# Performance work log

Measured on AMD Instinct MI355X. Metric: run time of the kernel, lower is better.

## Reference

```python
import math
import jax, jax.numpy as jnp
import numpy as np

B, R, L_, K_, U_ = 64, 32, 64, 16, 4
DIMS = [2 * K_ * U_, 256, 256, K_]  # [input_dim] + hidden_dim + [output_dim]
BN_EPS = 1e-5


def _uniform_param(key, out_dim, in_dim):
    ini = math.sqrt(3.0 / out_dim / in_dim)
    return jax.random.uniform(key, (out_dim, in_dim), jnp.float32, -ini, ini)


def setup_inputs() -> dict:
    key = jax.random.key(0)
    ks = jax.random.split(key, 16)
    inp = {
        "Hhat_real": jax.random.normal(ks[0], (B, R, L_, K_, U_), jnp.float32),
        "Hhat_imag": jax.random.normal(ks[1], (B, R, L_, K_, U_), jnp.float32),
        "Vhat": jax.random.normal(ks[2], (B, R, L_, K_, U_), jnp.float32),
    }
    kidx = 3
    for i in range(len(DIMS) - 1):
        inp[f"P1_{i}"] = _uniform_param(ks[kidx], DIMS[i + 1], DIMS[i]); kidx += 1
        inp[f"P2_{i}"] = _uniform_param(ks[kidx], DIMS[i + 1], DIMS[i]); kidx += 1
        if i != len(DIMS) - 2:  # BN only on non-final layers
            inp[f"bn_w{i}"] = jnp.ones((DIMS[i + 1],), jnp.float32)
            inp[f"bn_b{i}"] = jnp.zeros((DIMS[i + 1],), jnp.float32)
    inp["nbrOfRealizations"] = R
    inp["L"] = L_
    inp["K"] = K_
    inp["U"] = U_
    return inp


def _layer(A, P1, P2, bn_w, bn_b, relu):
    # A: [N, C_in, L]
    A1 = jnp.einsum('oc,ncl->nol', P1, A)                       # [N, C_out, L]
    A2 = jnp.einsum('oc,nc->no', P2, A.mean(-1))[:, :, None]    # [N, C_out, 1]
    A = A1 + 0.1 * A2
    if relu:
        A = jax.nn.relu(A)
    if bn_w is not None:
        # BatchNorm1d (training mode): normalize over (N, L) per channel
        mu = A.mean(axis=(0, 2), keepdims=True)
        var = A.var(axis=(0, 2), keepdims=True)
        A = (A - mu) * jax.lax.rsqrt(var + BN_EPS) * bn_w[None, :, None] + bn_b[None, :, None]
    return A


def reference(Hhat_real, Hhat_imag, Vhat,
              P1_0, P2_0, bn_w0, bn_b0,
              P1_1, P2_1, bn_w1, bn_b1,
              P1_2, P2_2,
              nbrOfRealizations, L, K, U):
    Bsz = Hhat_real.shape[0]
    N = Bsz * nbrOfRealizations

    def prep(X):
        # view(N,1,L,K,U).transpose(2,3).transpose(3,4) -> [N,1,K,U,L]
        return jnp.transpose(X.reshape(N, 1, L, K, U), (0, 1, 3, 4, 2))

    A = jnp.concatenate([prep(Hhat_real), prep(Hhat_imag)], axis=1).reshape(N, 2 * K * U, L)
    A = _layer(A, P1_0, P2_0, bn_w0, bn_b0, relu=True)
    A = _layer(A, P1_1, P2_1, bn_w1, bn_b1, relu=True)
    A = _layer(A, P1_2, P2_2, None, None, relu=False)

    Phat_u1 = jnp.transpose(A.reshape(Bsz, nbrOfRealizations, K, L), (0, 1, 3, 2))  # [B,R,L,K]
    nrm = jnp.linalg.norm(Phat_u1, axis=2, keepdims=True)                            # [B,R,1,K]
    Phat_u = Phat_u1 / nrm * jnp.float32(math.sqrt(L))
    Fhat_u = Vhat.reshape(Bsz, nbrOfRealizations, L, K, U) * Phat_u[..., None]
    return Fhat_u
```

## Files before the change

### kernel.cpp

```cpp
#include <hip/hip_runtime.h>

typedef unsigned short ushort_t;
typedef unsigned int uint_t;

typedef short bf16x8 __attribute__((ext_vector_type(8)));
typedef float f32x4 __attribute__((ext_vector_type(4)));
#define MFMA16(a, b, c) __builtin_amdgcn_mfma_f32_16x16x32_bf16(a, b, c, 0, 0, 0)

__device__ __forceinline__ float bf2f(uint_t u) { return __uint_as_float(u << 16); }
__device__ __forceinline__ ushort_t f2bf(float f) {
  uint_t x = __float_as_uint(f);
  return (ushort_t)((x + 0x7fffu + ((x >> 16) & 1u)) >> 16);
}
__device__ __forceinline__ uint_t cvtpk(float lo, float hi) {
  uint_t r;
  asm("v_cvt_pk_bf16_f32 %0, %1, %2" : "=v"(r) : "v"(lo), "v"(hi));
  return r;
}
__device__ __forceinline__ void gload_lds16(const void* g, void* l) {
  __builtin_amdgcn_global_load_lds(
      (const __attribute__((address_space(1))) unsigned int*)g,
      (__attribute__((address_space(3))) unsigned int*)l, 16, 0, 0);
}

#define NBATCH 2048

__global__ __launch_bounds__(256) void cvt_w0_kernel(
    const float* __restrict__ P1_0, ushort_t* __restrict__ W0bf)
{
  int i = blockIdx.x * 256 + threadIdx.x;
  W0bf[i] = f2bf(P1_0[i]);
}

__global__ __launch_bounds__(256) void pre0_kernel(
    const float* __restrict__ Hr, const float* __restrict__ Hi,
    const float* __restrict__ P2_0, float* __restrict__ V20)
{
  __shared__ float r[4][128];
  __shared__ float hm[128];
  const int t = threadIdx.x, n = blockIdx.x;
  const int q = t >> 6;
  const int c = (2 * t) & 127;
  const int cc = c & 63;
  const float* src = ((c < 64) ? Hr : Hi) + (size_t)n * 4096 + cc;
  float s0 = 0.f, s1 = 0.f;
  #pragma unroll
  for (int i = 0; i < 16; i++) {
    int l = 4 * i + q;
    float2 x = *(const float2*)(src + l * 64);
    s0 += x.x; s1 += x.y;
  }
  r[q][c] = s0; r[q][c + 1] = s1;
  __syncthreads();
  if (t < 128) hm[t] = (r[0][t] + r[1][t] + r[2][t] + r[3][t]) * (1.0f / 64.0f);
  __syncthreads();
  const float4* pw = (const float4*)(P2_0 + t * 128);
  float s = 0.f;
  #pragma unroll 8
  for (int c4 = 0; c4 < 32; c4++) {
    float4 p = pw[c4];
    s = fmaf(p.x, hm[4 * c4 + 0], s);
    s = fmaf(p.y, hm[4 * c4 + 1], s);
    s = fmaf(p.z, hm[4 * c4 + 2], s);
    s = fmaf(p.w, hm[4 * c4 + 3], s);
  }
  V20[n * 256 + t] = 0.1f * s;
}

__global__ __launch_bounds__(256) void layer0_mfma_kernel(
    const float* __restrict__ Hr, const float* __restrict__ Hi,
    const ushort_t* __restrict__ W0bf, const float* __restrict__ V20,
    ushort_t* __restrict__ Z, float* __restrict__ partA, float* __restrict__ partB)
{
  __shared__ ushort_t lds[64 * 264];
  const int t = threadIdx.x, n = blockIdx.x;
  const int lane = t & 63, w = t >> 6, r16 = lane & 15, g4 = lane >> 4;

  #pragma unroll
  for (int i = 0; i < 8; i++) {
    int idx = i * 1024 + t * 4;
    int p = idx >> 12;
    int r = idx & 4095;
    int l = r >> 6, c = r & 63;
    const float* src = (p ? Hi : Hr) + (size_t)n * 4096 + r;
    float4 x = *(const float4*)src;
    uint2 pr = make_uint2(cvtpk(x.x, x.y), cvtpk(x.z, x.w));
    *(uint2*)(&lds[l * 136 + p * 64 + c]) = pr;
  }

  float4 v2r[4];
  #pragma unroll
  for (int m = 0; m < 4; m++)
    v2r[m] = *(const float4*)(V20 + n * 256 + w * 64 + m * 16 + g4 * 4);

  f32x4 acc[4][4];
  #pragma unroll
  for (int i = 0; i < 4; i++)
    #pragma unroll
    for (int j = 0; j < 4; j++) acc[i][j] = (f32x4){0.f, 0.f, 0.f, 0.f};

  __syncthreads();
  #pragma unroll
  for (int kk = 0; kk < 4; kk++) {
    bf16x8 aF[4], bF[4];
    #pragma unroll
    for (int m = 0; m < 4; m++)
      aF[m] = *(const bf16x8*)(W0bf + (w * 64 + m * 16 + r16) * 128 + kk * 32 + g4 * 8);
    #pragma unroll
    for (int nt = 0; nt < 4; nt++)
      bF[nt] = *(const bf16x8*)(&lds[(nt * 16 + r16) * 136 + kk * 32 + g4 * 8]);
    #pragma unroll
    for (int m = 0; m < 4; m++)
      #pragma unroll
      for (int nt = 0; nt < 4; nt++)
        acc[m][nt] = MFMA16(aF[m], bF[nt], acc[m][nt]);
  }

  #pragma unroll
  for (int m = 0; m < 4; m++) {
    float s[4] = {0.f, 0.f, 0.f, 0.f}, q[4] = {0.f, 0.f, 0.f, 0.f};
    #pragma unroll
    for (int nt = 0; nt < 4; nt++)
      #pragma unroll
      for (int r = 0; r < 4; r++) {
        float v = fmaxf(acc[m][nt][r] + v2r[m][r], 0.f);
        s[r] += v; q[r] = fmaf(v, v, q[r]);
      }
    #pragma unroll
    for (int b = 1; b < 16; b <<= 1)
      #pragma unroll
      for (int r = 0; r < 4; r++) {
        s[r] += __shfl_xor(s[r], b);
        q[r] += __shfl_xor(q[r], b);
      }
    const int ob = w * 64 + m * 16 + g4 * 4;
    #pragma unroll
    for (int r = 0; r < 4; r++)
      if (r16 == r) {
        partA[n * 256 + ob + r] = s[r];
        partB[n * 256 + ob + r] = q[r];
      }
  }

  __syncthreads();
  #pragma unroll
  for (int m = 0; m < 4; m++) {
    const int ob = w * 64 + m * 16 + g4 * 4;
    #pragma unroll
    for (int nt = 0; nt < 4; nt++) {
      const int l = nt * 16 + r16;
      uint_t p0 = cvtpk(fmaxf(acc[m][nt][0] + v2r[m].x, 0.f),
                        fmaxf(acc[m][nt][1] + v2r[m].y, 0.f));
      uint_t p1 = cvtpk(fmaxf(acc[m][nt][2] + v2r[m].z, 0.f),
                        fmaxf(acc[m][nt][3] + v2r[m].w, 0.f));
      *(uint2*)(&lds[l * 264 + ob]) = make_uint2(p0, p1);
    }
  }
  __syncthreads();
  #pragma unroll
  for (int i = 0; i < 8; i++) {
    int el = i * 2048 + t * 8;
    int l = el >> 8, o0 = el & 255;
    *(uint4*)(&Z[(size_t)n * 16384 + el]) = *(const uint4*)(&lds[l * 264 + o0]);
  }
}

__global__ __launch_bounds__(256) void statsfin_kernel(
    const float* __restrict__ partA, const float* __restrict__ partB,
    const float* __restrict__ bnw, const float* __restrict__ bnb,
    float* __restrict__ stats)
{
  __shared__ float s1s[256], s2s[256];
  const int c = blockIdx.x, t = threadIdx.x;
  float s1 = 0.f, s2 = 0.f;
  #pragma unroll
  for (int j = 0; j < 8; j++) {
    int n = t * 8 + j;
    s1 += partA[n * 256 + c];
    s2 += partB[n * 256 + c];
  }
  s1s[t] = s1; s2s[t] = s2;
  __syncthreads();
  for (int s = 128; s > 0; s >>= 1) {
    if (t < s) { s1s[t] += s1s[t + s]; s2s[t] += s2s[t + s]; }
    __syncthreads();
  }
  if (t == 0) {
    const float inv = 1.0f / 131072.0f;
    float mu = s1s[0] * inv;
    float var = fmaxf(s2s[0] * inv - mu * mu, 0.f);
    float rstd = rsqrtf(var + 1e-5f);
    float sc = rstd * bnw[c];
    stats[2 * c]     = sc;
    stats[2 * c + 1] = bnb[c] - mu * sc;
  }
}

__global__ __launch_bounds__(256) void prep_kernel(
    const float* __restrict__ P1f, const float* __restrict__ P2f,
    const float* __restrict__ stats, ushort_t* __restrict__ Wbf,
    float* __restrict__ P2s, float* __restrict__ biasT)
{
  const int o = blockIdx.x, t = threadIdx.x;
  float sc = stats[2 * t], sh = stats[2 * t + 1];
  float w = P1f[o * 256 + t];
  Wbf[o * 256 + t] = f2bf(w * sc);
  float p = P2f[o * 256 + t];
  P2s[o * 256 + t] = p * sc;
  __shared__ float s1[256], s2[256];
  s1[t] = w * sh;
  s2[t] = p * sh;
  __syncthreads();
  for (int s = 128; s > 0; s >>= 1) {
    if (t < s) { s1[t] += s1[t + s]; s2[t] += s2[t + s]; }
    __syncthreads();
  }
  if (t == 0) biasT[o] = s1[0] + 0.1f * s2[0];
}

__global__ __launch_bounds__(256) void v2n_kernel(
    const float* __restrict__ partA, const float* __restrict__ P2s,
    const float* __restrict__ biasT, float* __restrict__ V2)
{
  __shared__ float zm[4][256];
  const int t = threadIdx.x, n0 = blockIdx.x * 4;
  #pragma unroll
  for (int j = 0; j < 4; j++) zm[j][t] = partA[(n0 + j) * 256 + t] * (1.0f / 64.0f);
  __syncthreads();
  float s[4] = {0.f, 0.f, 0.f, 0.f};
  const float4* pw = (const float4*)(P2s + t * 256);
  #pragma unroll 4
  for (int c4 = 0; c4 < 64; c4++) {
    float4 p = pw[c4];
    #pragma unroll
    for (int j = 0; j < 4; j++) {
      s[j] = fmaf(p.x, zm[j][4 * c4 + 0], s[j]);
      s[j] = fmaf(p.y, zm[j][4 * c4 + 1], s[j]);
      s[j] = fmaf(p.z, zm[j][4 * c4 + 2], s[j]);
      s[j] = fmaf(p.w, zm[j][4 * c4 + 3], s[j]);
    }
  }
  float b = biasT[t];
  #pragma unroll
  for (int j = 0; j < 4; j++) V2[(n0 + j) * 256 + t] = 0.1f * s[j] + b;
}

__global__ __launch_bounds__(256) void v2w_kernel(
    const float* __restrict__ partA, const float* __restrict__ P2s2,
    const float* __restrict__ biasT2, float* __restrict__ V22)
{
  __shared__ float zm[256];
  __shared__ float red[16][17];
  const int t = threadIdx.x, n = blockIdx.x;
  zm[t] = partA[n * 256 + t] * (1.0f / 64.0f);
  __syncthreads();
  const int oi = t & 15, ch = t >> 4;
  const float4* pw = (const float4*)(P2s2 + oi * 256 + ch * 16);
  float s = 0.f;
  #pragma unroll
  for (int c4 = 0; c4 < 4; c4++) {
    float4 p = pw[c4];
    int cb = ch * 16 + c4 * 4;
    s = fmaf(p.x, zm[cb + 0], s);
    s = fmaf(p.y, zm[cb + 1], s);
    s = fmaf(p.z, zm[cb + 2], s);
    s = fmaf(p.w, zm[cb + 3], s);
  }
  red[ch][oi] = s;
  __syncthreads();
  if (t < 16) {
    float acc = 0.f;
    #pragma unroll
    for (int c = 0; c < 16; c++) acc += red[c][t];
    V22[n * 16 + t] = 0.1f * acc + biasT2[t];
  }
}

__global__ __launch_bounds__(256) void layer1_mfma_kernel(
    ushort_t* Z, const ushort_t* __restrict__ W1bf, const float* __restrict__ V21,
    float* __restrict__ partA, float* __restrict__ partB)
{
  __shared__ ushort_t lds[64 * 264];
  const int t = threadIdx.x, n = blockIdx.x;
  const int lane = t & 63, w = t >> 6, r16 = lane & 15, g4 = lane >> 4;
  const size_t zbase = (size_t)n * 16384;

  #pragma unroll
  for (int i = 0; i < 8; i++) {
    int G = (w * 8 + i) * 64 + lane;
    int row = G >> 5;
    int gc = G & 31;
    int gsrc = gc ^ (row & 7);
    gload_lds16(Z + zbase + row * 256 + gsrc * 8, &lds[(w * 8 + i) * 512]);
  }

  float4 v2r[4];
  #pragma unroll
  for (int m = 0; m < 4; m++)
    v2r[m] = *(const float4*)(V21 + n * 256 + w * 64 + m * 16 + g4 * 4);

  f32x4 acc[4][4];
  #pragma unroll
  for (int i = 0; i < 4; i++)
    #pragma unroll
    for (int j = 0; j < 4; j++) acc[i][j] = (f32x4){0.f, 0.f, 0.f, 0.f};

  bf16x8 aF[2][4];
  #pragma unroll
  for (int m = 0; m < 4; m++)
    aF[0][m] = *(const bf16x8*)(W1bf + (w * 64 + m * 16 + r16) * 256 + g4 * 8);

  __syncthreads();

  const int sw = r16 & 7;
  #pragma unroll
  for (int kk = 0; kk < 8; kk++) {
    const int cur = kk & 1, nxt = cur ^ 1;
    if (kk < 7) {
      #pragma unroll
      for (int m = 0; m < 4; m++)
        aF[nxt][m] = *(const bf16x8*)(W1bf + (w * 64 + m * 16 + r16) * 256 + (kk + 1) * 32 + g4 * 8);
    }
    bf16x8 bF[4];
    #pragma unroll
    for (int nt = 0; nt < 4; nt++) {
      const int row = nt * 16 + r16;
      bF[nt] = *(const bf16x8*)(&lds[row * 256 + (((kk * 4 + g4) ^ sw) * 8)]);
    }
    #pragma unroll
    for (int m = 0; m < 4; m++)
      #pragma unroll
      for (int nt = 0; nt < 4; nt++)
        acc[m][nt] = MFMA16(aF[cur][m], bF[nt], acc[m][nt]);
  }

  #pragma unroll
  for (int m = 0; m < 4; m++) {
    float s[4] = {0.f, 0.f, 0.f, 0.f}, q[4] = {0.f, 0.f, 0.f, 0.f};
    #pragma unroll
    for (int nt = 0; nt < 4; nt++)
      #pragma unroll
      for (int r = 0; r < 4; r++) {
        float v = fmaxf(acc[m][nt][r] + v2r[m][r], 0.f);
        s[r] += v; q[r] = fmaf(v, v, q[r]);
      }
    #pragma unroll
    for (int b = 1; b < 16; b <<= 1)
      #pragma unroll
      for (int r = 0; r < 4; r++) {
        s[r] += __shfl_xor(s[r], b);
        q[r] += __shfl_xor(q[r], b);
      }
    const int ob = w * 64 + m * 16 + g4 * 4;
    #pragma unroll
    for (int r = 0; r < 4; r++)
      if (r16 == r) {
        partA[n * 256 + ob + r] = s[r];
        partB[n * 256 + ob + r] = q[r];
      }
  }

  __syncthreads();
  #pragma unroll
  for (int m = 0; m < 4; m++) {
    const int ob = w * 64 + m * 16 + g4 * 4;
    #pragma unroll
    for (int nt = 0; nt < 4; nt++) {
      const int l = nt * 16 + r16;
      uint_t p0 = cvtpk(fmaxf(acc[m][nt][0] + v2r[m].x, 0.f),
                        fmaxf(acc[m][nt][1] + v2r[m].y, 0.f));
      uint_t p1 = cvtpk(fmaxf(acc[m][nt][2] + v2r[m].z, 0.f),
                        fmaxf(acc[m][nt][3] + v2r[m].w, 0.f));
      *(uint2*)(&lds[l * 264 + ob]) = make_uint2(p0, p1);
    }
  }
  __syncthreads();
  #pragma unroll
  for (int i = 0; i < 8; i++) {
    int el = i * 2048 + t * 8;
    int l = el >> 8, o0 = el & 255;
    *(uint4*)(&Z[zbase + el]) = *(const uint4*)(&lds[l * 264 + o0]);
  }
}

__global__ __launch_bounds__(256) void layer2final_kernel(
    const ushort_t* __restrict__ Z, const ushort_t* __restrict__ W2bf,
    const float* __restrict__ V22, const float* __restrict__ Vh,
    float* __restrict__ out)
{
  __shared__ float v2s[16];
  __shared__ float zf[16][65];
  __shared__ float invn[16];
  const int t = threadIdx.x, n = blockIdx.x;
  const int lane = t & 63, w = t >> 6, r16 = lane & 15, g4 = lane >> 4;
  const size_t zbase = (size_t)n * 16384;

  if (t < 16) v2s[t] = V22[n * 16 + t];

  f32x4 acc = (f32x4){0.f, 0.f, 0.f, 0.f};
  #pragma unroll 2
  for (int kk = 0; kk < 8; kk++) {
    bf16x8 aF = *(const bf16x8*)(W2bf + r16 * 256 + kk * 32 + g4 * 8);
    bf16x8 bF = *(const bf16x8*)(Z + zbase + (w * 16 + r16) * 256 + kk * 32 + g4 * 8);
    acc = MFMA16(aF, bF, acc);
  }
  __syncthreads();
  #pragma unroll
  for (int r = 0; r < 4; r++) {
    int o = g4 * 4 + r;
    zf[o][w * 16 + r16] = acc[r] + v2s[o];
  }
  __syncthreads();
  if (t < 16) {
    float s = 0.f;
    #pragma unroll
    for (int l = 0; l < 64; l++) s = fmaf(zf[t][l], zf[t][l], s);
    invn[t] = (s > 0.f) ? (8.0f * rsqrtf(s)) : 0.f;
  }
  __syncthreads();
  const size_t base = (size_t)n * 4096;
  #pragma unroll
  for (int g = 0; g < 4; g++) {
    int e = t * 16 + g * 4;
    int l = e >> 6;
    int k = (e >> 2) & 15;
    float val = zf[k][l] * invn[k];
    float4 vv = *(const float4*)(Vh + base + e);
    *(float4*)(out + base + e) =
        make_float4(vv.x * val, vv.y * val, vv.z * val, vv.w * val);
  }
}

extern "C" void kernel_launch(void* const* d_in, const int* in_sizes, int n_in,
                              void* d_out, int out_size, void* d_ws, size_t ws_size,
                              hipStream_t stream) {
  const float* Hr   = (const float*)d_in[0];
  const float* Hi   = (const float*)d_in[1];
  const float* Vh   = (const float*)d_in[2];
  const float* P1_0 = (const float*)d_in[3];
  const float* P2_0 = (const float*)d_in[4];
  const float* bnw0 = (const float*)d_in[5];
  const float* bnb0 = (const float*)d_in[6];
  const float* P1_1 = (const float*)d_in[7];
  const float* P2_1 = (const float*)d_in[8];
  const float* bnw1 = (const float*)d_in[9];
  const float* bnb1 = (const float*)d_in[10];
  const float* P1_2 = (const float*)d_in[11];
  const float* P2_2 = (const float*)d_in[12];

  char* ws = (char*)d_ws;
  float*    stats0 = (float*)   (ws);
  float*    stats1 = (float*)   (ws + 2048);
  float*    biasT  = (float*)   (ws + 4096);
  float*    biasT2 = (float*)   (ws + 5120);
  ushort_t* W0bf   = (ushort_t*)(ws + 8192);
  ushort_t* W1bf   = (ushort_t*)(ws + 73728);
  ushort_t* W2bf   = (ushort_t*)(ws + 204800);
  float*    P2s1   = (float*)   (ws + 212992);
  float*    P2s2   = (float*)   (ws + 475136);
  float*    partA  = (float*)   (ws + 491520);
  float*    partB  = (float*)   (ws + 2588672);
  float*    V20    = (float*)   (ws + 4685824);
  float*    V21    = (float*)   (ws + 6782976);
  float*    V22    = (float*)   (ws + 8880128);
  ushort_t* Z      = (ushort_t*)(ws + 9437184);

  cvt_w0_kernel<<<128, 256, 0, stream>>>(P1_0, W0bf);
  pre0_kernel<<<NBATCH, 256, 0, stream>>>(Hr, Hi, P2_0, V20);
  layer0_mfma_kernel<<<NBATCH, 256, 0, stream>>>(Hr, Hi, W0bf, V20, Z, partA, partB);
  statsfin_kernel<<<256, 256, 0, stream>>>(partA, partB, bnw0, bnb0, stats0);
  prep_kernel<<<256, 256, 0, stream>>>(P1_1, P2_1, stats0, W1bf, P2s1, biasT);
  v2n_kernel<<<512, 256, 0, stream>>>(partA, P2s1, biasT, V21);
  layer1_mfma_kernel<<<NBATCH, 256, 0, stream>>>(Z, W1bf, V21, partA, partB);
  statsfin_kernel<<<256, 256, 0, stream>>>(partA, partB, bnw1, bnb1, stats1);
  prep_kernel<<<16, 256, 0, stream>>>(P1_2, P2_2, stats1, W2bf, P2s2, biasT2);
  v2w_kernel<<<NBATCH, 256, 0, stream>>>(partA, P2s2, biasT2, V22);
  layer2final_kernel<<<NBATCH, 256, 0, stream>>>(Z, W2bf, V22, Vh, (float*)d_out);
}
```

Measured before the change: 212.5 us.

## Fuse small kernels and stage layer-0 input via direct global-to-LDS loads

Folds the P1_0 bf16 conversion into pre0_kernel and the per-sample layer-2 mean projection (v2w) into layer2final_kernel, removing two launches and the V22 round trip through global memory. Layer 0 now copies fp32 Hhat into LDS with a swizzled global_load_lds instead of register loads, and converts to bf16 when the MFMA B fragments are read. This trades a doubled LDS footprint in fp32 and repeated per-fragment conversion for less register staging and asynchronous loads.

```diff
diff --git a/kernel.cpp b/kernel.cpp
--- a/kernel.cpp
+++ b/kernel.cpp
@@ -25,20 +25,18 @@
 
 #define NBATCH 2048
 
-__global__ __launch_bounds__(256) void cvt_w0_kernel(
-    const float* __restrict__ P1_0, ushort_t* __restrict__ W0bf)
-{
-  int i = blockIdx.x * 256 + threadIdx.x;
-  W0bf[i] = f2bf(P1_0[i]);
-}
-
 __global__ __launch_bounds__(256) void pre0_kernel(
     const float* __restrict__ Hr, const float* __restrict__ Hi,
-    const float* __restrict__ P2_0, float* __restrict__ V20)
+    const float* __restrict__ P2_0, const float* __restrict__ P1_0,
+    ushort_t* __restrict__ W0bf, float* __restrict__ V20)
 {
   __shared__ float r[4][128];
   __shared__ float hm[128];
   const int t = threadIdx.x, n = blockIdx.x;
+  if (n < 128) {
+    int i = n * 256 + t;
+    W0bf[i] = f2bf(P1_0[i]);
+  }
   const int q = t >> 6;
   const int c = (2 * t) & 127;
   const int cc = c & 63;
@@ -72,20 +70,20 @@
     const ushort_t* __restrict__ W0bf, const float* __restrict__ V20,
     ushort_t* __restrict__ Z, float* __restrict__ partA, float* __restrict__ partB)
 {
-  __shared__ ushort_t lds[64 * 264];
+  __shared__ __align__(16) ushort_t lds[64 * 264];
+  float* ldsf = (float*)lds;
   const int t = threadIdx.x, n = blockIdx.x;
   const int lane = t & 63, w = t >> 6, r16 = lane & 15, g4 = lane >> 4;
 
   #pragma unroll
   for (int i = 0; i < 8; i++) {
-    int idx = i * 1024 + t * 4;
-    int p = idx >> 12;
-    int r = idx & 4095;
-    int l = r >> 6, c = r & 63;
-    const float* src = (p ? Hi : Hr) + (size_t)n * 4096 + r;
-    float4 x = *(const float4*)src;
-    uint2 pr = make_uint2(cvtpk(x.x, x.y), cvtpk(x.z, x.w));
-    *(uint2*)(&lds[l * 136 + p * 64 + c]) = pr;
+    int G = (w * 8 + i) * 64 + lane;
+    int row = G >> 5;
+    int gc = G & 31;
+    int gsrc = gc ^ (row & 7);
+    int fi = gsrc * 4;
+    const float* src = ((fi < 64) ? Hr : Hi) + (size_t)n * 4096 + row * 64 + (fi & 63);
+    gload_lds16(src, &ldsf[(w * 8 + i) * 256]);
   }
 
   float4 v2r[4];
@@ -100,6 +98,8 @@
     for (int j = 0; j < 4; j++) acc[i][j] = (f32x4){0.f, 0.f, 0.f, 0.f};
 
   __syncthreads();
+
+  const int sw = r16 & 7;
   #pragma unroll
   for (int kk = 0; kk < 4; kk++) {
     bf16x8 aF[4], bF[4];
@@ -107,8 +107,16 @@
     for (int m = 0; m < 4; m++)
       aF[m] = *(const bf16x8*)(W0bf + (w * 64 + m * 16 + r16) * 128 + kk * 32 + g4 * 8);
     #pragma unroll
-    for (int nt = 0; nt < 4; nt++)
-      bF[nt] = *(const bf16x8*)(&lds[(nt * 16 + r16) * 136 + kk * 32 + g4 * 8]);
+    for (int nt = 0; nt < 4; nt++) {
+      const int row = nt * 16 + r16;
+      const float* base = ldsf + row * 128;
+      const int g0 = kk * 8 + g4 * 2;
+      float4 xa = *(const float4*)(base + ((g0 ^ sw) * 4));
+      float4 xb = *(const float4*)(base + (((g0 + 1) ^ sw) * 4));
+      uint4 u = make_uint4(cvtpk(xa.x, xa.y), cvtpk(xa.z, xa.w),
+                           cvtpk(xb.x, xb.y), cvtpk(xb.z, xb.w));
+      bF[nt] = *(const bf16x8*)&u;
+    }
     #pragma unroll
     for (int m = 0; m < 4; m++)
       #pragma unroll
@@ -245,42 +253,11 @@
   for (int j = 0; j < 4; j++) V2[(n0 + j) * 256 + t] = 0.1f * s[j] + b;
 }
 
-__global__ __launch_bounds__(256) void v2w_kernel(
-    const float* __restrict__ partA, const float* __restrict__ P2s2,
-    const float* __restrict__ biasT2, float* __restrict__ V22)
-{
-  __shared__ float zm[256];
-  __shared__ float red[16][17];
-  const int t = threadIdx.x, n = blockIdx.x;
-  zm[t] = partA[n * 256 + t] * (1.0f / 64.0f);
-  __syncthreads();
-  const int oi = t & 15, ch = t >> 4;
-  const float4* pw = (const float4*)(P2s2 + oi * 256 + ch * 16);
-  float s = 0.f;
-  #pragma unroll
-  for (int c4 = 0; c4 < 4; c4++) {
-    float4 p = pw[c4];
-    int cb = ch * 16 + c4 * 4;
-    s = fmaf(p.x, zm[cb + 0], s);
-    s = fmaf(p.y, zm[cb + 1], s);
-    s = fmaf(p.z, zm[cb + 2], s);
-    s = fmaf(p.w, zm[cb + 3], s);
-  }
-  red[ch][oi] = s;
-  __syncthreads();
-  if (t < 16) {
-    float acc = 0.f;
-    #pragma unroll
-    for (int c = 0; c < 16; c++) acc += red[c][t];
-    V22[n * 16 + t] = 0.1f * acc + biasT2[t];
-  }
-}
-
 __global__ __launch_bounds__(256) void layer1_mfma_kernel(
     ushort_t* Z, const ushort_t* __restrict__ W1bf, const float* __restrict__ V21,
     float* __restrict__ partA, float* __restrict__ partB)
 {
-  __shared__ ushort_t lds[64 * 264];
+  __shared__ __align__(16) ushort_t lds[64 * 264];
   const int t = threadIdx.x, n = blockIdx.x;
   const int lane = t & 63, w = t >> 6, r16 = lane & 15, g4 = lane >> 4;
   const size_t zbase = (size_t)n * 16384;
@@ -385,9 +362,12 @@
 
 __global__ __launch_bounds__(256) void layer2final_kernel(
     const ushort_t* __restrict__ Z, const ushort_t* __restrict__ W2bf,
-    const float* __restrict__ V22, const float* __restrict__ Vh,
+    const float* __restrict__ partA, const float* __restrict__ P2s2,
+    const float* __restrict__ biasT2, const float* __restrict__ Vh,
     float* __restrict__ out)
 {
+  __shared__ float zm[256];
+  __shared__ float red[16][17];
   __shared__ float v2s[16];
   __shared__ float zf[16][65];
   __shared__ float invn[16];
@@ -395,7 +375,7 @@
   const int lane = t & 63, w = t >> 6, r16 = lane & 15, g4 = lane >> 4;
   const size_t zbase = (size_t)n * 16384;
 
-  if (t < 16) v2s[t] = V22[n * 16 + t];
+  zm[t] = partA[n * 256 + t] * (1.0f / 64.0f);
 
   f32x4 acc = (f32x4){0.f, 0.f, 0.f, 0.f};
   #pragma unroll 2
@@ -403,6 +383,29 @@
     bf16x8 aF = *(const bf16x8*)(W2bf + r16 * 256 + kk * 32 + g4 * 8);
     bf16x8 bF = *(const bf16x8*)(Z + zbase + (w * 16 + r16) * 256 + kk * 32 + g4 * 8);
     acc = MFMA16(aF, bF, acc);
+  }
+  __syncthreads();
+  {
+    const int oi = t & 15, ch = t >> 4;
+    const float4* pw = (const float4*)(P2s2 + oi * 256 + ch * 16);
+    float s = 0.f;
+    #pragma unroll
+    for (int c4 = 0; c4 < 4; c4++) {
+      float4 p = pw[c4];
+      int cb = ch * 16 + c4 * 4;
+      s = fmaf(p.x, zm[cb + 0], s);
+      s = fmaf(p.y, zm[cb + 1], s);
+      s = fmaf(p.z, zm[cb + 2], s);
+      s = fmaf(p.w, zm[cb + 3], s);
+    }
+    red[ch][oi] = s;
+  }
+  __syncthreads();
+  if (t < 16) {
+    float a = 0.f;
+    #pragma unroll
+    for (int c = 0; c < 16; c++) a += red[c][t];
+    v2s[t] = 0.1f * a + biasT2[t];
   }
   __syncthreads();
   #pragma unroll
@@ -462,11 +465,9 @@
   float*    partB  = (float*)   (ws + 2588672);
   float*    V20    = (float*)   (ws + 4685824);
   float*    V21    = (float*)   (ws + 6782976);
-  float*    V22    = (float*)   (ws + 8880128);
   ushort_t* Z      = (ushort_t*)(ws + 9437184);
 
-  cvt_w0_kernel<<<128, 256, 0, stream>>>(P1_0, W0bf);
-  pre0_kernel<<<NBATCH, 256, 0, stream>>>(Hr, Hi, P2_0, V20);
+  pre0_kernel<<<NBATCH, 256, 0, stream>>>(Hr, Hi, P2_0, P1_0, W0bf, V20);
   layer0_mfma_kernel<<<NBATCH, 256, 0, stream>>>(Hr, Hi, W0bf, V20, Z, partA, partB);
   statsfin_kernel<<<256, 256, 0, stream>>>(partA, partB, bnw0, bnb0, stats0);
   prep_kernel<<<256, 256, 0, stream>>>(P1_1, P2_1, stats0, W1bf, P2s1, biasT);
@@ -474,6 +475,5 @@
   layer1_mfma_kernel<<<NBATCH, 256, 0, stream>>>(Z, W1bf, V21, partA, partB);
   statsfin_kernel<<<256, 256, 0, stream>>>(partA, partB, bnw1, bnb1, stats1);
   prep_kernel<<<16, 256, 0, stream>>>(P1_2, P2_2, stats1, W2bf, P2s2, biasT2);
-  v2w_kernel<<<NBATCH, 256, 0, stream>>>(partA, P2s2, biasT2, V22);
-  layer2final_kernel<<<NBATCH, 256, 0, stream>>>(Z, W2bf, V22, Vh, (float*)d_out);
-}
+  layer2final_kernel<<<NBATCH, 256, 0, stream>>>(Z, W2bf, partA, P2s2, biasT2, Vh, (float*)d_out);
+}
```

Measured after the change: 206.7 us. -2.7%, faster.
